# Optimization experiments

Measured on AMD Instinct MI355X. Metric: run time of the kernel, lower is better.

Reference implementation:

```python
import jax, jax.numpy as jnp
import numpy as np

B, N = 1024, 32768


def setup_inputs() -> dict:
    key = jax.random.key(0)
    k1, k2 = jax.random.split(key)
    outputs = jax.random.normal(k1, (B, N), dtype=jnp.float32)
    # reference pulse rates in Hz, inside the pulse band (40/60, 250/60) Hz
    u = jax.random.uniform(k2, (B, 1), dtype=jnp.float32)
    targets = 0.8 + 3.1 * u
    return {"outputs": outputs, "targets": targets, "Fs": 20}


def reference(outputs, targets, Fs):
    n = outputs.shape[-1]
    nf = n // 2 + 1
    f = jnp.linspace(0.0, Fs / 2.0, nf, dtype=jnp.float32)  # (F,)
    min_idx = jnp.argmin(jnp.abs(f - 40.0 / 60.0))
    max_idx = jnp.argmin(jnp.abs(f - 250.0 / 60.0))

    # torch.rfft(..., normalized=True) == orthonormal rFFT; P1 = |X|^2
    X = jnp.fft.rfft(outputs, norm="ortho")  # (B, F) complex
    P1 = X.real ** 2 + X.imag ** 2  # (B, F)

    # per-sample nearest freq bin to the reference rate
    ref_idx = jnp.argmin(jnp.abs(f[None, :] - targets), axis=1)  # (B,)

    idx = jnp.arange(nf)[None, :]  # (1, F)
    r = ref_idx[:, None]  # (B, 1)
    # slices [min_idx : ref_idx-1] and [ref_idx+2 : max_idx]
    mask = ((idx >= min_idx) & (idx < r - 1)) | ((idx >= r + 2) & (idx < max_idx))
    denom = (max_idx - min_idx - 3).astype(jnp.float32)
    other_avg = jnp.sum(P1 * mask, axis=1) / denom  # (B,)

    pulse_amp = jnp.take_along_axis(P1, ref_idx[:, None], axis=1)[:, 0]  # (B,)
    losses = -10.0 * jnp.log10(pulse_amp / other_avg)
    return jnp.mean(losses)
```

## Files before the change

### kernel.cpp

```cpp
#include <hip/hip_runtime.h>
#include <hip/hip_fp16.h>
#include <math.h>

#define BROWS 1024
#define NPTS  32768
#define MPTS  16384
#define NTHR  512
#define MIN_IDX 1092
#define MAX_IDX 6827
#define DENOMF  5732.0f


#define LDH 136
#define PLN (128 * LDH)

typedef _Float16 h8 __attribute__((ext_vector_type(8)));
typedef float    f4 __attribute__((ext_vector_type(4)));

#define MFMA(a, b, c) __builtin_amdgcn_mfma_f32_16x16x32_f16((a), (b), (c), 0, 0, 0)

#define ANG128 (-0.04908738521234052f)
#define ANG16K (-3.834951969714103e-4f)
#define ANG32K (-1.9174759848570515e-4f)
#define GRC 0.9951847266721969f
#define GRS (-0.09801714032956060f)


__device__ inline h8 ldf(const __half* p) {
    return *reinterpret_cast<const h8*>(p);
}

__device__ inline float bin_pow(const __half2* __restrict__ C, int k,
                                float c, float sn) {
    float2 a  = __half22float2(C[(k >> 7) * LDH + (k & 127)]);
    int p = MPTS - k;
    float2 bz = __half22float2(C[(p >> 7) * LDH + (p & 127)]);
    float bx = bz.x, by = -bz.y;
    float ex = 0.5f * (a.x + bx), ey = 0.5f * (a.y + by);
    float dx = a.x - bx,          dy = a.y - by;
    float ox = 0.5f * dy,         oy = -0.5f * dx;
    float Xx = ex + ox * c - oy * sn;
    float Xy = ey + ox * sn + oy * c;
    return (Xx * Xx + Xy * Xy) * (1.0f / (float)NPTS);
}

__device__ inline float bin_pow_sc(const __half2* __restrict__ C, int k) {
    float c, sn;
    __sincosf(ANG32K * (float)k, &sn, &c);
    return bin_pow(C, k, c, sn);
}

__global__ __launch_bounds__(NTHR, 4) void snr_row_kernel(
        const float* __restrict__ outs,
        const float* __restrict__ targets,
        float* __restrict__ row_loss) {
    __shared__ __align__(16) __half pl[2 * PLN];
    __shared__ float red[NTHR / 64];

    const int b    = blockIdx.x;
    const int tid  = threadIdx.x;
    const int lane = tid & 63;
    const int w    = tid >> 6;
    const int r15  = lane & 15;
    const int g    = lane >> 4;
    const float2* row = reinterpret_cast<const float2*>(outs + (size_t)b * NPTS);

    #pragma unroll
    for (int it = 0; it < MPTS / NTHR; ++it) {
        int m = tid + it * NTHR;
        float2 v = row[m];
        int idx = (m & 127) * LDH + (m >> 7);
        pl[idx]       = (__half)v.x;
        pl[PLN + idx] = (__half)v.y;
    }

    h8 fr[4], fi[4];
    {
        const int frow = 16 * w + r15;
        float stc, sts;
        __sincosf(ANG128 * (float)frow, &sts, &stc);
        #pragma unroll
        for (int kc = 0; kc < 4; ++kc) {
            int e0 = (frow * (32 * kc + 8 * g)) & 127;
            float c, s;
            __sincosf(ANG128 * (float)e0, &s, &c);
            #pragma unroll
            for (int j = 0; j < 8; ++j) {
                fr[kc][j] = (_Float16)c;
                fi[kc][j] = (_Float16)s;
                float nc = c * stc - s * sts;
                s = c * sts + s * stc;
                c = nc;
            }
        }
    }
    __syncthreads();

    float tc[4], ts[4], uc[4], us[4];
    #pragma unroll
    for (int v = 0; v < 4; ++v) {
        int k1 = 16 * w + 4 * g + v;
        __sincosf(ANG16K * (float)(k1 * r15), &ts[v], &tc[v]);
        __sincosf(ANG16K * (float)(16 * k1), &us[v], &uc[v]);
    }

    __half2 bm[8][4];
    #pragma unroll
    for (int n0 = 0; n0 < 8; ++n0) {
        f4 accr = {0.f, 0.f, 0.f, 0.f}, acci = {0.f, 0.f, 0.f, 0.f};
        #pragma unroll
        for (int kc = 0; kc < 4; ++kc) {
            int base = (16 * n0 + r15) * LDH + 32 * kc + 8 * g;
            h8 zr = ldf(&pl[base]);
            h8 zi = ldf(&pl[PLN + base]);
            h8 fin = -fi[kc];
            accr = MFMA(fr[kc], zr, accr);
            accr = MFMA(fin,    zi, accr);
            acci = MFMA(fr[kc], zi, acci);
            acci = MFMA(fi[kc], zr, acci);
        }
        #pragma unroll
        for (int v = 0; v < 4; ++v) {
            float br = accr[v] * tc[v] - acci[v] * ts[v];
            float bi = accr[v] * ts[v] + acci[v] * tc[v];
            bm[n0][v] = __floats2half2_rn(br, bi);
            float nc = tc[v] * uc[v] - ts[v] * us[v];
            ts[v] = tc[v] * us[v] + ts[v] * uc[v];
            tc[v] = nc;
        }
    }
    __syncthreads();

    #pragma unroll
    for (int n0 = 0; n0 < 8; ++n0)
        #pragma unroll
        for (int v = 0; v < 4; ++v) {
            int idx = (16 * w + 4 * g + v) * LDH + 16 * n0 + r15;
            pl[idx]       = __low2half(bm[n0][v]);
            pl[PLN + idx] = __high2half(bm[n0][v]);
        }
    __syncthreads();

    __half2 ct[8][4];
    #pragma unroll
    for (int m0 = 0; m0 < 8; ++m0) {
        f4 accr = {0.f, 0.f, 0.f, 0.f}, acci = {0.f, 0.f, 0.f, 0.f};
        #pragma unroll
        for (int kc = 0; kc < 4; ++kc) {
            int base = (16 * m0 + r15) * LDH + 32 * kc + 8 * g;
            h8 ar = ldf(&pl[base]);
            h8 ai = ldf(&pl[PLN + base]);
            h8 ain = -ai;
            accr = MFMA(ar,  fr[kc], accr);
            accr = MFMA(ain, fi[kc], accr);
            acci = MFMA(ar,  fi[kc], acci);
            acci = MFMA(ai,  fr[kc], acci);
        }
        #pragma unroll
        for (int v = 0; v < 4; ++v)
            ct[m0][v] = __floats2half2_rn(accr[v], acci[v]);
    }
    __syncthreads();

    __half2* C = reinterpret_cast<__half2*>(pl);
    #pragma unroll
    for (int m0 = 0; m0 < 8; ++m0)
        #pragma unroll
        for (int v = 0; v < 4; ++v)
            C[(16 * w + r15) * LDH + 16 * m0 + 4 * g + v] = ct[m0][v];
    __syncthreads();

    float local = 0.0f;
    {
        int k = MIN_IDX + tid;
        float cc, ss;
        __sincosf(ANG32K * (float)k, &ss, &cc);
        for (; k < MAX_IDX; k += NTHR) {
            local += bin_pow(C, k, cc, ss);
            float nc = cc * GRC - ss * GRS;
            ss = cc * GRS + ss * GRC;
            cc = nc;
        }
    }
    for (int off = 32; off; off >>= 1) local += __shfl_down(local, off);
    if ((tid & 63) == 0) red[w] = local;
    __syncthreads();

    if (tid == 0) {
        float S = 0.0f;
        #pragma unroll
        for (int q = 0; q < NTHR / 64; ++q) S += red[q];

        float tgt = targets[b];
        double kd = (double)tgt * (16384.0 / 10.0);
        int k0 = (int)kd;
        const float stepf = 10.0f / 16384.0f;
        float f0 = (float)k0 * stepf;
        float f1 = (float)(k0 + 1) * stepf;
        float d0 = fabsf(f0 - tgt);
        float d1 = fabsf(f1 - tgt);
        int rr = (d0 <= d1) ? k0 : (k0 + 1);

        float pm1 = bin_pow_sc(C, rr - 1);
        float p0  = bin_pow_sc(C, rr);
        float pp1 = bin_pow_sc(C, rr + 1);
        float other_avg = (S - pm1 - p0 - pp1) * (1.0f / DENOMF);
        row_loss[b] = -10.0f * log10f(p0 / other_avg);
    }
}

__global__ __launch_bounds__(256) void snr_reduce_kernel(
        const float* __restrict__ row_loss, float* __restrict__ out) {
    __shared__ float red[4];
    float s = 0.0f;
    for (int i = threadIdx.x; i < BROWS; i += 256) s += row_loss[i];
    for (int off = 32; off; off >>= 1) s += __shfl_down(s, off);
    if ((threadIdx.x & 63) == 0) red[threadIdx.x >> 6] = s;
    __syncthreads();
    if (threadIdx.x == 0)
        out[0] = (red[0] + red[1] + red[2] + red[3]) * (1.0f / (float)BROWS);
}

extern "C" void kernel_launch(void* const* d_in, const int* in_sizes, int n_in,
                              void* d_out, int out_size, void* d_ws, size_t ws_size,
                              hipStream_t stream) {
    const float* outs    = (const float*)d_in[0];
    const float* targets = (const float*)d_in[1];
    float* ws  = (float*)d_ws;
    float* out = (float*)d_out;

    snr_row_kernel<<<BROWS, NTHR, 0, stream>>>(outs, targets, ws);
    snr_reduce_kernel<<<1, 256, 0, stream>>>(ws, out);
}
```

Baseline: 66.34 us.

## Double block threads, load DFT twiddles from global table, split tiles across wave halves

Result: slower. 80.14 us (+20.8%).

```diff
diff --git a/kernel.cpp b/kernel.cpp
--- a/kernel.cpp
+++ b/kernel.cpp
@@ -5,7 +5,7 @@
 #define BROWS 1024
 #define NPTS  32768
 #define MPTS  16384
-#define NTHR  512
+#define NTHR  1024
 #define MIN_IDX 1092
 #define MAX_IDX 6827
 #define DENOMF  5732.0f
@@ -22,8 +22,6 @@
 #define ANG128 (-0.04908738521234052f)
 #define ANG16K (-3.834951969714103e-4f)
 #define ANG32K (-1.9174759848570515e-4f)
-#define GRC 0.9951847266721969f
-#define GRS (-0.09801714032956060f)
 
 
 __device__ inline h8 ldf(const __half* p) {
@@ -50,9 +48,19 @@
     return bin_pow(C, k, c, sn);
 }
 
+__global__ __launch_bounds__(256) void finit_kernel(__half* __restrict__ Ft) {
+    int i = blockIdx.x * 256 + threadIdx.x;
+    int r = i >> 7, c = i & 127;
+    float s, co;
+    __sincosf(ANG128 * (float)((r * c) & 127), &s, &co);
+    Ft[i]         = (__half)co;
+    Ft[16384 + i] = (__half)s;
+}
+
 __global__ __launch_bounds__(NTHR, 4) void snr_row_kernel(
         const float* __restrict__ outs,
         const float* __restrict__ targets,
+        const __half* __restrict__ Ft,
         float* __restrict__ row_loss) {
     __shared__ __align__(16) __half pl[2 * PLN];
     __shared__ float red[NTHR / 64];
@@ -61,6 +69,8 @@
     const int tid  = threadIdx.x;
     const int lane = tid & 63;
     const int w    = tid >> 6;
+    const int p    = w & 7;
+    const int h    = w >> 3;
     const int r15  = lane & 15;
     const int g    = lane >> 4;
     const float2* row = reinterpret_cast<const float2*>(outs + (size_t)b * NPTS);
@@ -73,117 +83,90 @@
         pl[idx]       = (__half)v.x;
         pl[PLN + idx] = (__half)v.y;
     }
-
-    h8 fr[4], fi[4];
-    {
-        const int frow = 16 * w + r15;
-        float stc, sts;
-        __sincosf(ANG128 * (float)frow, &sts, &stc);
-        #pragma unroll
-        for (int kc = 0; kc < 4; ++kc) {
-            int e0 = (frow * (32 * kc + 8 * g)) & 127;
-            float c, s;
-            __sincosf(ANG128 * (float)e0, &s, &c);
-            #pragma unroll
-            for (int j = 0; j < 8; ++j) {
-                fr[kc][j] = (_Float16)c;
-                fi[kc][j] = (_Float16)s;
-                float nc = c * stc - s * sts;
-                s = c * sts + s * stc;
-                c = nc;
-            }
-        }
-    }
-    __syncthreads();
-
-    float tc[4], ts[4], uc[4], us[4];
-    #pragma unroll
-    for (int v = 0; v < 4; ++v) {
-        int k1 = 16 * w + 4 * g + v;
-        __sincosf(ANG16K * (float)(k1 * r15), &ts[v], &tc[v]);
-        __sincosf(ANG16K * (float)(16 * k1), &us[v], &uc[v]);
-    }
-
-    __half2 bm[8][4];
-    #pragma unroll
-    for (int n0 = 0; n0 < 8; ++n0) {
+    __syncthreads();
+
+    const __half* FrB = Ft + (16 * p + r15) * 128;
+    const __half* FiB = Ft + 16384 + (16 * p + r15) * 128;
+
+    __half2 bm[4][4];
+    #pragma unroll
+    for (int i = 0; i < 4; ++i) {
+        const int n0 = 4 * h + i;
         f4 accr = {0.f, 0.f, 0.f, 0.f}, acci = {0.f, 0.f, 0.f, 0.f};
         #pragma unroll
         for (int kc = 0; kc < 4; ++kc) {
             int base = (16 * n0 + r15) * LDH + 32 * kc + 8 * g;
             h8 zr = ldf(&pl[base]);
             h8 zi = ldf(&pl[PLN + base]);
-            h8 fin = -fi[kc];
-            accr = MFMA(fr[kc], zr, accr);
-            accr = MFMA(fin,    zi, accr);
-            acci = MFMA(fr[kc], zi, acci);
-            acci = MFMA(fi[kc], zr, acci);
+            h8 fr = ldf(&FrB[32 * kc + 8 * g]);
+            h8 fi = ldf(&FiB[32 * kc + 8 * g]);
+            h8 fin = -fi;
+            accr = MFMA(fr,  zr, accr);
+            accr = MFMA(fin, zi, accr);
+            acci = MFMA(fr,  zi, acci);
+            acci = MFMA(fi,  zr, acci);
         }
         #pragma unroll
         for (int v = 0; v < 4; ++v) {
-            float br = accr[v] * tc[v] - acci[v] * ts[v];
-            float bi = accr[v] * ts[v] + acci[v] * tc[v];
-            bm[n0][v] = __floats2half2_rn(br, bi);
-            float nc = tc[v] * uc[v] - ts[v] * us[v];
-            ts[v] = tc[v] * us[v] + ts[v] * uc[v];
-            tc[v] = nc;
-        }
-    }
-    __syncthreads();
-
-    #pragma unroll
-    for (int n0 = 0; n0 < 8; ++n0)
+            int k1 = 16 * p + 4 * g + v;
+            int n2 = 16 * n0 + r15;
+            int e  = (k1 * n2) & 16383;
+            float s, c;
+            __sincosf(ANG16K * (float)e, &s, &c);
+            bm[i][v] = __floats2half2_rn(accr[v] * c - acci[v] * s,
+                                         accr[v] * s + acci[v] * c);
+        }
+    }
+    __syncthreads();
+
+    #pragma unroll
+    for (int i = 0; i < 4; ++i)
         #pragma unroll
         for (int v = 0; v < 4; ++v) {
-            int idx = (16 * w + 4 * g + v) * LDH + 16 * n0 + r15;
-            pl[idx]       = __low2half(bm[n0][v]);
-            pl[PLN + idx] = __high2half(bm[n0][v]);
-        }
-    __syncthreads();
-
-    __half2 ct[8][4];
-    #pragma unroll
-    for (int m0 = 0; m0 < 8; ++m0) {
+            int idx = (16 * p + 4 * g + v) * LDH + 16 * (4 * h + i) + r15;
+            pl[idx]       = __low2half(bm[i][v]);
+            pl[PLN + idx] = __high2half(bm[i][v]);
+        }
+    __syncthreads();
+
+    __half2 ct[4][4];
+    #pragma unroll
+    for (int i = 0; i < 4; ++i) {
+        const int m0 = 4 * h + i;
         f4 accr = {0.f, 0.f, 0.f, 0.f}, acci = {0.f, 0.f, 0.f, 0.f};
         #pragma unroll
         for (int kc = 0; kc < 4; ++kc) {
             int base = (16 * m0 + r15) * LDH + 32 * kc + 8 * g;
             h8 ar = ldf(&pl[base]);
             h8 ai = ldf(&pl[PLN + base]);
+            h8 fr = ldf(&FrB[32 * kc + 8 * g]);
+            h8 fi = ldf(&FiB[32 * kc + 8 * g]);
             h8 ain = -ai;
-            accr = MFMA(ar,  fr[kc], accr);
-            accr = MFMA(ain, fi[kc], accr);
-            acci = MFMA(ar,  fi[kc], acci);
-            acci = MFMA(ai,  fr[kc], acci);
+            accr = MFMA(ar,  fr, accr);
+            accr = MFMA(ain, fi, accr);
+            acci = MFMA(ar,  fi, acci);
+            acci = MFMA(ai,  fr, acci);
         }
         #pragma unroll
         for (int v = 0; v < 4; ++v)
-            ct[m0][v] = __floats2half2_rn(accr[v], acci[v]);
+            ct[i][v] = __floats2half2_rn(accr[v], acci[v]);
     }
     __syncthreads();
 
     __half2* C = reinterpret_cast<__half2*>(pl);
     #pragma unroll
-    for (int m0 = 0; m0 < 8; ++m0)
+    for (int i = 0; i < 4; ++i)
         #pragma unroll
         for (int v = 0; v < 4; ++v)
-            C[(16 * w + r15) * LDH + 16 * m0 + 4 * g + v] = ct[m0][v];
+            C[(16 * p + r15) * LDH + 16 * (4 * h + i) + 4 * g + v] = ct[i][v];
     __syncthreads();
 
     float local = 0.0f;
-    {
-        int k = MIN_IDX + tid;
-        float cc, ss;
-        __sincosf(ANG32K * (float)k, &ss, &cc);
-        for (; k < MAX_IDX; k += NTHR) {
-            local += bin_pow(C, k, cc, ss);
-            float nc = cc * GRC - ss * GRS;
-            ss = cc * GRS + ss * GRC;
-            cc = nc;
-        }
-    }
+    for (int k = MIN_IDX + tid; k < MAX_IDX; k += NTHR)
+        local += bin_pow_sc(C, k);
+
     for (int off = 32; off; off >>= 1) local += __shfl_down(local, off);
-    if ((tid & 63) == 0) red[w] = local;
+    if (lane == 0) red[w] = local;
     __syncthreads();
 
     if (tid == 0) {
@@ -226,9 +209,11 @@
                               hipStream_t stream) {
     const float* outs    = (const float*)d_in[0];
     const float* targets = (const float*)d_in[1];
-    float* ws  = (float*)d_ws;
+    float*  ws_loss = (float*)d_ws;
+    __half* Ft      = (__half*)((char*)d_ws + 4096);
     float* out = (float*)d_out;
 
-    snr_row_kernel<<<BROWS, NTHR, 0, stream>>>(outs, targets, ws);
-    snr_reduce_kernel<<<1, 256, 0, stream>>>(ws, out);
-}
+    finit_kernel<<<64, 256, 0, stream>>>(Ft);
+    snr_row_kernel<<<BROWS, NTHR, 0, stream>>>(outs, targets, Ft, ws_loss);
+    snr_reduce_kernel<<<1, 256, 0, stream>>>(ws_loss, out);
+}
```
